# Kernel optimization log

Measured on AMD Instinct MI355X. Metric: run time of the kernel, lower is better.

Reference implementation:

```python
import jax, jax.numpy as jnp
import numpy as np

B, K, D = 8192, 8192, 256

def setup_inputs() -> dict:
    key = jax.random.key(0)
    kz, ke = jax.random.split(key)
    z = jax.random.normal(kz, (B, D), dtype=jnp.float32)
    embeddings = jax.random.normal(ke, (K, D), dtype=jnp.float32)
    return {"z": z, "embeddings": embeddings}

def reference(z, embeddings):
    # Squared Euclidean distance via ||z||^2 + ||e||^2 - 2 z.e (same math as
    # the broadcasted (z - e)^2 sum, without the [B, K, D] intermediate).
    z_sq = jnp.sum(z * z, axis=1, keepdims=True)            # [B, 1]
    e_sq = jnp.sum(embeddings * embeddings, axis=1)         # [K]
    cross = jnp.einsum('bd,kd->bk', z, embeddings)          # [B, K]
    dist = z_sq + e_sq[None, :] - 2.0 * cross               # [B, K]
    idx = jnp.argmin(dist, axis=1)                          # [B]
    return embeddings[idx]                                  # [B, D]
```

## Files before the change

kernel.cpp:

```cpp
#include <hip/hip_runtime.h>
#include <hip/hip_bf16.h>
#include <stdint.h>


#define NB 8192
#define NK 8192
#define ND 256
#define NCHUNK (NK / 64)

typedef __attribute__((ext_vector_type(4))) _Float16 half4;
typedef __attribute__((ext_vector_type(8))) _Float16 half8;
typedef __attribute__((ext_vector_type(4))) float f32x4;

__device__ __forceinline__ unsigned int fkey(float f) {
  unsigned int i = __float_as_uint(f);
  return (i & 0x80000000u) ? ~i : (i | 0x80000000u);
}

__device__ __forceinline__ void gload_lds16(const void* g, void* l) {
  __builtin_amdgcn_global_load_lds(
      (const __attribute__((address_space(1))) unsigned int*)g,
      (__attribute__((address_space(3))) unsigned int*)l, 16, 0, 0);
}

__global__ __launch_bounds__(256) void prep_split(
    const float4* __restrict__ z4, const float4* __restrict__ e4,
    half4* __restrict__ zh, half4* __restrict__ zl,
    half4* __restrict__ eh, half4* __restrict__ el) {
  int i = blockIdx.x * 256 + threadIdx.x;
  const int NZ = (NB * ND) / 4;
  const float4* s;
  half4 *dh, *dl;
  int j;
  if (i < NZ) { s = z4; dh = zh; dl = zl; j = i; }
  else        { s = e4; dh = eh; dl = el; j = i - NZ; }
  float4 v = s[j];
  half4 h, l;
  h.x = (_Float16)v.x; l.x = (_Float16)((v.x - (float)h.x) * 2048.0f);
  h.y = (_Float16)v.y; l.y = (_Float16)((v.y - (float)h.y) * 2048.0f);
  h.z = (_Float16)v.z; l.z = (_Float16)((v.z - (float)h.z) * 2048.0f);
  h.w = (_Float16)v.w; l.w = (_Float16)((v.w - (float)h.w) * 2048.0f);
  dh[j] = h;
  dl[j] = l;
}

__global__ __launch_bounds__(256) void esq_kernel(const float* __restrict__ e,
                                                  float* __restrict__ esq) {
  int row = blockIdx.x * 4 + (threadIdx.x >> 6);
  int lane = threadIdx.x & 63;
  float4 v = ((const float4*)(e + (size_t)row * ND))[lane];
  double s = (double)v.x * v.x + (double)v.y * v.y + (double)v.z * v.z +
             (double)v.w * v.w;
#pragma unroll
  for (int sh = 1; sh < 64; sh <<= 1) s += __shfl_xor(s, sh, 64);
  if (lane == 0) esq[row] = (float)s;
}

__global__ __launch_bounds__(256, 2) void gemm_argmin(
    const _Float16* __restrict__ zh, const _Float16* __restrict__ zl,
    const _Float16* __restrict__ eh, const _Float16* __restrict__ el,
    const float* __restrict__ esq, unsigned long long* __restrict__ cand) {
  __shared__ __align__(16) _Float16 sAh[128 * 32];
  __shared__ __align__(16) _Float16 sAl[128 * 32];
  __shared__ __align__(16) _Float16 sBh[128 * 32];
  __shared__ __align__(16) _Float16 sBl[128 * 32];
  const int tid = threadIdx.x;
  const int wave = tid >> 6, lane = tid & 63;
  const int bx = blockIdx.x, by = blockIdx.y;
  const int wr = wave >> 1, wc = wave & 1;
  const int row0 = by * 128, col0 = bx * 128;

  f32x4 acc1[4][4] = {};
  f32x4 acc2[4][4] = {};

  const int fr = lane & 15;
  const int fk = (lane >> 4) * 8;

  for (int ks = 0; ks < 8; ++ks) {
    const int kc = ks * 32;
    __syncthreads();
#pragma unroll
    for (int i = 0; i < 2; ++i) {
      const int base = wave * 128 + i * 64;
      const int chunk = base + lane;
      const int r = chunk >> 2, c8 = (chunk & 3) * 8;
      const size_t loff = (size_t)base * 8;
      gload_lds16(zh + (size_t)(row0 + r) * ND + kc + c8, sAh + loff);
      gload_lds16(zl + (size_t)(row0 + r) * ND + kc + c8, sAl + loff);
      gload_lds16(eh + (size_t)(col0 + r) * ND + kc + c8, sBh + loff);
      gload_lds16(el + (size_t)(col0 + r) * ND + kc + c8, sBl + loff);
    }
    __syncthreads();

    half8 ah[4], al[4], bh[4], bl[4];
#pragma unroll
    for (int m = 0; m < 4; ++m) {
      int r = wr * 64 + m * 16 + fr;
      ah[m] = *(const half8*)&sAh[r * 32 + fk];
      al[m] = *(const half8*)&sAl[r * 32 + fk];
    }
#pragma unroll
    for (int n = 0; n < 4; ++n) {
      int c = wc * 64 + n * 16 + fr;
      bh[n] = *(const half8*)&sBh[c * 32 + fk];
      bl[n] = *(const half8*)&sBl[c * 32 + fk];
    }
#pragma unroll
    for (int m = 0; m < 4; ++m)
#pragma unroll
      for (int n = 0; n < 4; ++n) {
        acc1[m][n] = __builtin_amdgcn_mfma_f32_16x16x32_f16(ah[m], bh[n], acc1[m][n], 0, 0, 0);
        acc2[m][n] = __builtin_amdgcn_mfma_f32_16x16x32_f16(ah[m], bl[n], acc2[m][n], 0, 0, 0);
        acc2[m][n] = __builtin_amdgcn_mfma_f32_16x16x32_f16(al[m], bh[n], acc2[m][n], 0, 0, 0);
      }
  }

  float es[4];
#pragma unroll
  for (int n = 0; n < 4; ++n) es[n] = esq[col0 + wc * 64 + n * 16 + fr];
  const int chunkIdx = bx * 2 + wc;
#pragma unroll
  for (int m = 0; m < 4; ++m) {
#pragma unroll
    for (int j = 0; j < 4; ++j) {
      unsigned long long best = ~0ull;
#pragma unroll
      for (int n = 0; n < 4; ++n) {
        float cross = acc1[m][n][j] + acc2[m][n][j] * (1.0f / 2048.0f);
        float dist = es[n] - 2.0f * cross;
        unsigned int col = col0 + wc * 64 + n * 16 + fr;
        unsigned long long p = ((unsigned long long)fkey(dist) << 32) | col;
        best = p < best ? p : best;
      }
#pragma unroll
      for (int s = 1; s < 16; s <<= 1) {
        unsigned long long o = __shfl_xor(best, s, 64);
        best = o < best ? o : best;
      }
      if ((lane & 15) == 0) {
        int row = row0 + wr * 64 + m * 16 + (lane >> 4) * 4 + j;
        cand[(size_t)row * NCHUNK + chunkIdx] = best;
      }
    }
  }
}

__global__ __launch_bounds__(256) void rerank(
    const unsigned long long* __restrict__ cand, const float* __restrict__ z,
    const float* __restrict__ e, float* __restrict__ out) {
  const int row = blockIdx.x;
  const int tid = threadIdx.x, wave = tid >> 6, lane = tid & 63;
  __shared__ unsigned long long sc[NCHUNK];
  __shared__ int sidx[4];
  __shared__ double sdist[4];
  __shared__ int sbest;
  if (tid < NCHUNK) sc[tid] = cand[(size_t)row * NCHUNK + tid];
  __syncthreads();
  if (wave == 0) {
    unsigned long long v0 = sc[lane], v1 = sc[lane + 64];
    for (int r = 0; r < 4; ++r) {
      unsigned long long mn = v0 < v1 ? v0 : v1;
#pragma unroll
      for (int s = 1; s < 64; s <<= 1) {
        unsigned long long o = __shfl_xor(mn, s, 64);
        mn = o < mn ? o : mn;
      }
      if (lane == 0) sidx[r] = (int)(mn & 0xFFFFFFFFu);
      if (v0 == mn) v0 = ~0ull;
      if (v1 == mn) v1 = ~0ull;
    }
  }
  __syncthreads();
  {
    int idx = sidx[wave];
    double s = 0.0;
#pragma unroll
    for (int t = 0; t < 4; ++t) {
      int d = lane * 4 + t;
      double diff = (double)z[(size_t)row * ND + d] - (double)e[(size_t)idx * ND + d];
      s += diff * diff;
    }
#pragma unroll
    for (int sh = 1; sh < 64; sh <<= 1) s += __shfl_xor(s, sh, 64);
    if (lane == 0) sdist[wave] = s;
  }
  __syncthreads();
  if (tid == 0) {
    double bd = sdist[0];
    int bi = sidx[0];
    for (int w = 1; w < 4; ++w) {
      if (sdist[w] < bd || (sdist[w] == bd && sidx[w] < bi)) { bd = sdist[w]; bi = sidx[w]; }
    }
    sbest = bi;
  }
  __syncthreads();
  out[(size_t)row * ND + tid] = e[(size_t)sbest * ND + tid];
}

extern "C" void kernel_launch(void* const* d_in, const int* in_sizes, int n_in,
                              void* d_out, int out_size, void* d_ws, size_t ws_size,
                              hipStream_t stream) {
  const float* z = (const float*)d_in[0];
  const float* e = (const float*)d_in[1];
  float* out = (float*)d_out;
  char* ws = (char*)d_ws;

  _Float16* zh = (_Float16*)ws;
  _Float16* zl = zh + (size_t)NB * ND;
  _Float16* eh = zl + (size_t)NB * ND;
  _Float16* el = eh + (size_t)NK * ND;
  float* esq = (float*)(ws + 16u * 1024 * 1024);
  unsigned long long* cand =
      (unsigned long long*)(ws + 16u * 1024 * 1024 + 65536);

  prep_split<<<((NB + NK) * ND / 4) / 256, 256, 0, stream>>>(
      (const float4*)z, (const float4*)e, (half4*)zh, (half4*)zl, (half4*)eh,
      (half4*)el);
  esq_kernel<<<NK / 4, 256, 0, stream>>>(e, esq);
  gemm_argmin<<<dim3(NK / 128, NB / 128), 256, 0, stream>>>(zh, zl, eh, el, esq, cand);
  rerank<<<NB, 256, 0, stream>>>(cand, z, e, out);
}
```

Baseline: 219.0 us.

## Drop fp16 split-precision GEMM, keep top-2 per chunk with exact rerank

```diff
diff --git a/kernel.cpp b/kernel.cpp
--- a/kernel.cpp
+++ b/kernel.cpp
@@ -11,6 +11,7 @@
 typedef __attribute__((ext_vector_type(4))) _Float16 half4;
 typedef __attribute__((ext_vector_type(8))) _Float16 half8;
 typedef __attribute__((ext_vector_type(4))) float f32x4;
+typedef unsigned long long u64;
 
 __device__ __forceinline__ unsigned int fkey(float f) {
   unsigned int i = __float_as_uint(f);
@@ -23,97 +24,94 @@
       (__attribute__((address_space(3))) unsigned int*)l, 16, 0, 0);
 }
 
-__global__ __launch_bounds__(256) void prep_split(
-    const float4* __restrict__ z4, const float4* __restrict__ e4,
-    half4* __restrict__ zh, half4* __restrict__ zl,
-    half4* __restrict__ eh, half4* __restrict__ el) {
-  int i = blockIdx.x * 256 + threadIdx.x;
-  const int NZ = (NB * ND) / 4;
-  const float4* s;
-  half4 *dh, *dl;
-  int j;
-  if (i < NZ) { s = z4; dh = zh; dl = zl; j = i; }
-  else        { s = e4; dh = eh; dl = el; j = i - NZ; }
-  float4 v = s[j];
-  half4 h, l;
-  h.x = (_Float16)v.x; l.x = (_Float16)((v.x - (float)h.x) * 2048.0f);
-  h.y = (_Float16)v.y; l.y = (_Float16)((v.y - (float)h.y) * 2048.0f);
-  h.z = (_Float16)v.z; l.z = (_Float16)((v.z - (float)h.z) * 2048.0f);
-  h.w = (_Float16)v.w; l.w = (_Float16)((v.w - (float)h.w) * 2048.0f);
-  dh[j] = h;
-  dl[j] = l;
-}
-
-__global__ __launch_bounds__(256) void esq_kernel(const float* __restrict__ e,
-                                                  float* __restrict__ esq) {
+__device__ __forceinline__ void top2_ins(u64 v, u64& b1, u64& b2) {
+  if (v < b1) { b2 = b1; b1 = v; }
+  else if (v < b2) { b2 = v; }
+}
+
+__device__ __forceinline__ void top2_merge(int s, u64& b1, u64& b2) {
+  u64 p1 = __shfl_xor(b1, s, 64);
+  u64 p2 = __shfl_xor(b2, s, 64);
+  u64 hi = b1 > p1 ? b1 : p1;
+  u64 lo2 = b2 < p2 ? b2 : p2;
+  b1 = b1 < p1 ? b1 : p1;
+  b2 = hi < lo2 ? hi : lo2;
+}
+
+__global__ __launch_bounds__(256) void prep(const float4* __restrict__ z4,
+                                            const float4* __restrict__ e4,
+                                            half4* __restrict__ zh,
+                                            half4* __restrict__ eh,
+                                            float* __restrict__ esq) {
   int row = blockIdx.x * 4 + (threadIdx.x >> 6);
   int lane = threadIdx.x & 63;
-  float4 v = ((const float4*)(e + (size_t)row * ND))[lane];
-  double s = (double)v.x * v.x + (double)v.y * v.y + (double)v.z * v.z +
-             (double)v.w * v.w;
-#pragma unroll
-  for (int sh = 1; sh < 64; sh <<= 1) s += __shfl_xor(s, sh, 64);
-  if (lane == 0) esq[row] = (float)s;
-}
-
-__global__ __launch_bounds__(256, 2) void gemm_argmin(
-    const _Float16* __restrict__ zh, const _Float16* __restrict__ zl,
-    const _Float16* __restrict__ eh, const _Float16* __restrict__ el,
-    const float* __restrict__ esq, unsigned long long* __restrict__ cand) {
-  __shared__ __align__(16) _Float16 sAh[128 * 32];
-  __shared__ __align__(16) _Float16 sAl[128 * 32];
-  __shared__ __align__(16) _Float16 sBh[128 * 32];
-  __shared__ __align__(16) _Float16 sBl[128 * 32];
+  bool isE = row >= NB;
+  int r = isE ? row - NB : row;
+  float4 v = (isE ? e4 : z4)[(size_t)r * 64 + lane];
+  half4 h;
+  h.x = (_Float16)v.x;
+  h.y = (_Float16)v.y;
+  h.z = (_Float16)v.z;
+  h.w = (_Float16)v.w;
+  (isE ? eh : zh)[(size_t)r * 64 + lane] = h;
+  if (isE) {
+    double s = (double)v.x * v.x + (double)v.y * v.y + (double)v.z * v.z +
+               (double)v.w * v.w;
+#pragma unroll
+    for (int sh = 1; sh < 64; sh <<= 1) s += __shfl_xor(s, sh, 64);
+    if (lane == 0) esq[r] = (float)s;
+  }
+}
+
+__global__ __launch_bounds__(256) void gemm_argmin(
+    const _Float16* __restrict__ zh, const _Float16* __restrict__ eh,
+    const float* __restrict__ esq, ulonglong2* __restrict__ cand) {
+  __shared__ __align__(16) _Float16 sT[2][128 * 64];
   const int tid = threadIdx.x;
   const int wave = tid >> 6, lane = tid & 63;
   const int bx = blockIdx.x, by = blockIdx.y;
   const int wr = wave >> 1, wc = wave & 1;
   const int row0 = by * 128, col0 = bx * 128;
-
-  f32x4 acc1[4][4] = {};
-  f32x4 acc2[4][4] = {};
-
-  const int fr = lane & 15;
-  const int fk = (lane >> 4) * 8;
-
+  const int fr = lane & 15, g = lane >> 4;
+
+  f32x4 acc[4][4] = {};
+
+#define STAGE(buf, ks)                                                        \
+  {                                                                           \
+    const int kc = (ks) * 32;                                                 \
+    _Pragma("unroll") for (int i = 0; i < 4; ++i) {                           \
+      const int base = (wave * 4 + i) * 64;      \
+      const int L = base + lane;                                              \
+      const int r = L >> 3, pos = L & 7, c = pos ^ (r & 7);                   \
+      const _Float16* src = (c < 4)                                           \
+          ? zh + (size_t)(row0 + r) * ND + kc + c * 8                         \
+          : eh + (size_t)(col0 + r) * ND + kc + (c - 4) * 8;                  \
+      gload_lds16(src, &sT[buf][(size_t)base * 8]);                           \
+    }                                                                         \
+  }
+
+  STAGE(0, 0)
+  __syncthreads();
   for (int ks = 0; ks < 8; ++ks) {
-    const int kc = ks * 32;
-    __syncthreads();
-#pragma unroll
-    for (int i = 0; i < 2; ++i) {
-      const int base = wave * 128 + i * 64;
-      const int chunk = base + lane;
-      const int r = chunk >> 2, c8 = (chunk & 3) * 8;
-      const size_t loff = (size_t)base * 8;
-      gload_lds16(zh + (size_t)(row0 + r) * ND + kc + c8, sAh + loff);
-      gload_lds16(zl + (size_t)(row0 + r) * ND + kc + c8, sAl + loff);
-      gload_lds16(eh + (size_t)(col0 + r) * ND + kc + c8, sBh + loff);
-      gload_lds16(el + (size_t)(col0 + r) * ND + kc + c8, sBl + loff);
-    }
-    __syncthreads();
-
-    half8 ah[4], al[4], bh[4], bl[4];
+    const int buf = ks & 1;
+    if (ks + 1 < 8) STAGE(buf ^ 1, ks + 1)
+    half8 a[4], b[4];
 #pragma unroll
     for (int m = 0; m < 4; ++m) {
       int r = wr * 64 + m * 16 + fr;
-      ah[m] = *(const half8*)&sAh[r * 32 + fk];
-      al[m] = *(const half8*)&sAl[r * 32 + fk];
+      a[m] = *(const half8*)&sT[buf][r * 64 + (g ^ (r & 7)) * 8];
+      int rb = wc * 64 + m * 16 + fr;
+      b[m] = *(const half8*)&sT[buf][rb * 64 + (((4 + g) ^ (rb & 7))) * 8];
     }
 #pragma unroll
-    for (int n = 0; n < 4; ++n) {
-      int c = wc * 64 + n * 16 + fr;
-      bh[n] = *(const half8*)&sBh[c * 32 + fk];
-      bl[n] = *(const half8*)&sBl[c * 32 + fk];
-    }
-#pragma unroll
     for (int m = 0; m < 4; ++m)
 #pragma unroll
-      for (int n = 0; n < 4; ++n) {
-        acc1[m][n] = __builtin_amdgcn_mfma_f32_16x16x32_f16(ah[m], bh[n], acc1[m][n], 0, 0, 0);
-        acc2[m][n] = __builtin_amdgcn_mfma_f32_16x16x32_f16(ah[m], bl[n], acc2[m][n], 0, 0, 0);
-        acc2[m][n] = __builtin_amdgcn_mfma_f32_16x16x32_f16(al[m], bh[n], acc2[m][n], 0, 0, 0);
-      }
-  }
+      for (int n = 0; n < 4; ++n)
+        acc[m][n] =
+            __builtin_amdgcn_mfma_f32_16x16x32_f16(a[m], b[n], acc[m][n], 0, 0, 0);
+    __syncthreads();
+  }
+#undef STAGE
 
   float es[4];
 #pragma unroll
@@ -123,74 +121,70 @@
   for (int m = 0; m < 4; ++m) {
 #pragma unroll
     for (int j = 0; j < 4; ++j) {
-      unsigned long long best = ~0ull;
+      u64 b1 = ~0ull, b2 = ~0ull;
 #pragma unroll
       for (int n = 0; n < 4; ++n) {
-        float cross = acc1[m][n][j] + acc2[m][n][j] * (1.0f / 2048.0f);
-        float dist = es[n] - 2.0f * cross;
+        float dist = es[n] - 2.0f * acc[m][n][j];
         unsigned int col = col0 + wc * 64 + n * 16 + fr;
-        unsigned long long p = ((unsigned long long)fkey(dist) << 32) | col;
-        best = p < best ? p : best;
+        top2_ins(((u64)fkey(dist) << 32) | col, b1, b2);
       }
-#pragma unroll
-      for (int s = 1; s < 16; s <<= 1) {
-        unsigned long long o = __shfl_xor(best, s, 64);
-        best = o < best ? o : best;
-      }
-      if ((lane & 15) == 0) {
-        int row = row0 + wr * 64 + m * 16 + (lane >> 4) * 4 + j;
-        cand[(size_t)row * NCHUNK + chunkIdx] = best;
+      top2_merge(1, b1, b2);
+      top2_merge(2, b1, b2);
+      top2_merge(4, b1, b2);
+      top2_merge(8, b1, b2);
+      if (fr == 0) {
+        int row = row0 + wr * 64 + m * 16 + g * 4 + j;
+        ulonglong2 p;
+        p.x = b1;
+        p.y = b2;
+        cand[(size_t)row * NCHUNK + chunkIdx] = p;
       }
     }
   }
 }
 
-__global__ __launch_bounds__(256) void rerank(
-    const unsigned long long* __restrict__ cand, const float* __restrict__ z,
-    const float* __restrict__ e, float* __restrict__ out) {
+__global__ __launch_bounds__(256) void rerank(const u64* __restrict__ cand,
+                                              const float4* __restrict__ z4,
+                                              const float4* __restrict__ e4,
+                                              const float* __restrict__ e,
+                                              float* __restrict__ out) {
   const int row = blockIdx.x;
   const int tid = threadIdx.x, wave = tid >> 6, lane = tid & 63;
-  __shared__ unsigned long long sc[NCHUNK];
-  __shared__ int sidx[4];
-  __shared__ double sdist[4];
+  __shared__ double sdist[8];
+  __shared__ int sidx[8];
   __shared__ int sbest;
-  if (tid < NCHUNK) sc[tid] = cand[(size_t)row * NCHUNK + tid];
-  __syncthreads();
-  if (wave == 0) {
-    unsigned long long v0 = sc[lane], v1 = sc[lane + 64];
-    for (int r = 0; r < 4; ++r) {
-      unsigned long long mn = v0 < v1 ? v0 : v1;
-#pragma unroll
-      for (int s = 1; s < 64; s <<= 1) {
-        unsigned long long o = __shfl_xor(mn, s, 64);
-        mn = o < mn ? o : mn;
-      }
-      if (lane == 0) sidx[r] = (int)(mn & 0xFFFFFFFFu);
-      if (v0 == mn) v0 = ~0ull;
-      if (v1 == mn) v1 = ~0ull;
+
+  u64 b1 = cand[(size_t)row * 256 + tid], b2 = ~0ull;
+#pragma unroll
+  for (int s = 1; s < 64; s <<= 1) top2_merge(s, b1, b2);
+  const int c1 = (int)(b1 & 0xFFFFFFFFu), c2 = (int)(b2 & 0xFFFFFFFFu);
+
+  float4 zv = z4[(size_t)row * 64 + lane];
+#pragma unroll
+  for (int t = 0; t < 2; ++t) {
+    int idx = t ? c2 : c1;
+    float4 ev = e4[(size_t)idx * 64 + lane];
+    double dx = (double)zv.x - (double)ev.x;
+    double dy = (double)zv.y - (double)ev.y;
+    double dz = (double)zv.z - (double)ev.z;
+    double dw = (double)zv.w - (double)ev.w;
+    double s = dx * dx + dy * dy + dz * dz + dw * dw;
+#pragma unroll
+    for (int sh = 1; sh < 64; sh <<= 1) s += __shfl_xor(s, sh, 64);
+    if (lane == 0) {
+      sdist[wave * 2 + t] = s;
+      sidx[wave * 2 + t] = idx;
     }
-  }
-  __syncthreads();
-  {
-    int idx = sidx[wave];
-    double s = 0.0;
-#pragma unroll
-    for (int t = 0; t < 4; ++t) {
-      int d = lane * 4 + t;
-      double diff = (double)z[(size_t)row * ND + d] - (double)e[(size_t)idx * ND + d];
-      s += diff * diff;
-    }
-#pragma unroll
-    for (int sh = 1; sh < 64; sh <<= 1) s += __shfl_xor(s, sh, 64);
-    if (lane == 0) sdist[wave] = s;
   }
   __syncthreads();
   if (tid == 0) {
     double bd = sdist[0];
     int bi = sidx[0];
-    for (int w = 1; w < 4; ++w) {
-      if (sdist[w] < bd || (sdist[w] == bd && sidx[w] < bi)) { bd = sdist[w]; bi = sidx[w]; }
-    }
+    for (int w = 1; w < 8; ++w)
+      if (sdist[w] < bd || (sdist[w] == bd && sidx[w] < bi)) {
+        bd = sdist[w];
+        bi = sidx[w];
+      }
     sbest = bi;
   }
   __syncthreads();
@@ -206,17 +200,13 @@
   char* ws = (char*)d_ws;
 
   _Float16* zh = (_Float16*)ws;
-  _Float16* zl = zh + (size_t)NB * ND;
-  _Float16* eh = zl + (size_t)NB * ND;
-  _Float16* el = eh + (size_t)NK * ND;
-  float* esq = (float*)(ws + 16u * 1024 * 1024);
-  unsigned long long* cand =
-      (unsigned long long*)(ws + 16u * 1024 * 1024 + 65536);
-
-  prep_split<<<((NB + NK) * ND / 4) / 256, 256, 0, stream>>>(
-      (const float4*)z, (const float4*)e, (half4*)zh, (half4*)zl, (half4*)eh,
-      (half4*)el);
-  esq_kernel<<<NK / 4, 256, 0, stream>>>(e, esq);
-  gemm_argmin<<<dim3(NK / 128, NB / 128), 256, 0, stream>>>(zh, zl, eh, el, esq, cand);
-  rerank<<<NB, 256, 0, stream>>>(cand, z, e, out);
-}
+  _Float16* eh = zh + (size_t)NB * ND;
+  float* esq = (float*)(ws + 8u * 1024 * 1024);
+  ulonglong2* cand = (ulonglong2*)(ws + 8u * 1024 * 1024 + 65536);
+
+  prep<<<(NB + NK) / 4, 256, 0, stream>>>((const float4*)z, (const float4*)e,
+                                          (half4*)zh, (half4*)eh, esq);
+  gemm_argmin<<<dim3(NK / 128, NB / 128), 256, 0, stream>>>(zh, eh, esq, cand);
+  rerank<<<NB, 256, 0, stream>>>((const u64*)cand, (const float4*)z,
+                                 (const float4*)e, e, out);
+}
```

Result: slower. 356.9 us (+63.0%).
